# Kernel tuning notes

Measured on AMD Instinct MI355X. Metric: run time of the kernel, lower is better.

## Reference

```python
import jax, jax.numpy as jnp
import numpy as np

N_TYPES = 7
DT = 0.1
TAU_INIT = 20.0


def setup_inputs() -> dict:
    key = jax.random.key(0)
    k0, k1, k2, k3 = jax.random.split(key, 4)
    N = 49000          # n_neurons, divisible by 7 types
    E = 1_600_000      # n_edges (~avg degree 32)
    B = 8              # batch (via explicit v_init)
    n_tm1 = N // N_TYPES
    type_ids = (jnp.arange(N) % N_TYPES).astype(jnp.int32)   # type 0 == 'Tm1'
    tm1_indices = jnp.arange(0, N, N_TYPES, dtype=jnp.int32)  # positions where type_ids==0
    return {
        "tm1_input": jax.random.normal(k0, (B, n_tm1), jnp.float32),
        "v_init": jnp.zeros((B, N), jnp.float32),
        "weights": jax.random.normal(k1, (E,), jnp.float32),
        "bias": jnp.zeros((N,), jnp.float32),
        "tau_params": jnp.full((N_TYPES,), TAU_INIT, jnp.float32),
        "scale_excitatory": jnp.ones((), jnp.float32),
        "scale_inhibitory": jnp.ones((), jnp.float32),
        "source_indices": jax.random.randint(k2, (E,), 0, N, dtype=jnp.int32),
        "target_indices": jax.random.randint(k3, (E,), 0, N, dtype=jnp.int32),
        "type_ids": type_ids,
        "tm1_indices": tm1_indices,
        "steps": 100,
    }


def reference(tm1_input, v_init, weights, bias, tau_params,
              scale_excitatory, scale_inhibitory,
              source_indices, target_indices, type_ids, tm1_indices, steps):
    # per-neuron tau from per-type params (torch: get_tau_vector via masks)
    tau = tau_params[type_ids]                                   # [N]
    one = jnp.ones((), weights.dtype)
    edge_scales = jnp.where(weights > 0, scale_excitatory,
                            jnp.where(weights < 0, scale_inhibitory, one))
    scaled_weights = weights * edge_scales                       # [E]

    def step(v, _):
        v = v.at[:, tm1_indices].set(tm1_input)                  # clamp Tm1 neurons
        r = jax.nn.relu(v)                                       # activation
        edge_currents = r[:, source_indices] * scaled_weights    # gather [B,E]
        syn = jnp.zeros_like(v).at[:, target_indices].add(edge_currents)  # scatter-add [B,N]
        dv = (-v + syn + bias) / tau
        dv = dv.at[:, tm1_indices].set(0.0)                      # Tm1 held fixed
        return v + DT * dv, None

    v, _ = jax.lax.scan(step, v_init, None, length=steps)
    return v
```

## Files before the change

### kernel.cpp

```cpp
#include <hip/hip_runtime.h>


#define BLK 256
#define STEPS 100
#define NBATCH 8
#define PRE 6
#define NBUCK 256
#define CHUNK 4096
#define PERT 16
static constexpr float DT_C = 0.1f;

typedef unsigned uv4 __attribute__((ext_vector_type(4)));

__device__ __forceinline__ unsigned f2bf_rne(float x) {
    unsigned u = __float_as_uint(x);
    return (u + 0x7FFFu + ((u >> 16) & 1u)) >> 16;
}
__device__ __forceinline__ unsigned pk_bf2(float a, float b) {
    return f2bf_rne(a) | (f2bf_rne(b) << 16);
}

__global__ void k_zero(int* counts, int* countS, int* tm1_pos, int N) {
    int i = blockIdx.x * BLK + threadIdx.x;
    if (i < N) { counts[i] = 0; countS[i] = 0; tm1_pos[i] = -1; }
}

__global__ void k_tm1pos(const int* __restrict__ tm1_idx, int* tm1_pos, int NT) {
    int i = blockIdx.x * BLK + threadIdx.x;
    if (i < NT) tm1_pos[tm1_idx[i]] = i;
}

__global__ void k_hist(const int* __restrict__ srcI, const int* __restrict__ tgt,
                       const int* __restrict__ type_ids,
                       int* counts, int* countS, unsigned char* __restrict__ flagA,
                       int E) {
    int i = blockIdx.x * BLK + threadIdx.x;
    if (i >= E) return;
    int t = tgt[i];
    atomicAdd(&counts[t], 1);
    unsigned char st = (type_ids[srcI[i]] == 0) ? 1 : 0;
    if (st) atomicAdd(&countS[t], 1);
    flagA[i] = st;
}

__global__ void k_scan1(const int* __restrict__ counts, int* offsets, int* bsum, int N) {
    __shared__ int s[BLK];
    int tx = threadIdx.x;
    int i = blockIdx.x * BLK + tx;
    int v = (i < N) ? counts[i] : 0;
    s[tx] = v; __syncthreads();
    for (int d = 1; d < BLK; d <<= 1) {
        int t = (tx >= d) ? s[tx - d] : 0;
        __syncthreads();
        s[tx] += t;
        __syncthreads();
    }
    if (i < N) offsets[i] = s[tx] - v;
    if (tx == BLK - 1) bsum[blockIdx.x] = s[tx];
}

__global__ void k_scan2(int* bsum, int nb) {
    __shared__ int s[BLK];
    int tx = threadIdx.x;
    int v = (tx < nb) ? bsum[tx] : 0;
    s[tx] = v; __syncthreads();
    for (int d = 1; d < BLK; d <<= 1) {
        int t = (tx >= d) ? s[tx - d] : 0;
        __syncthreads();
        s[tx] += t;
        __syncthreads();
    }
    if (tx < nb) bsum[tx] = s[tx] - v;
}

__global__ void k_scan3(const int* __restrict__ bsum, int* offsets, int N, int E) {
    int i = blockIdx.x * BLK + threadIdx.x;
    if (i < N) offsets[i] += bsum[i >> 8];
    else if (i == N) offsets[N] = E;
}

__global__ void k_prep(const int* __restrict__ offsets, const int* __restrict__ countS,
                       int* dynEnd, int* gCursor, int N, int span) {
    int i = blockIdx.x * BLK + threadIdx.x;
    if (i < N) dynEnd[i] = offsets[i + 1] - countS[i];
    if (i < NBUCK) {
        int t0 = i * span; if (t0 > N) t0 = N;
        gCursor[i] = offsets[t0];
    }
}

__global__ __launch_bounds__(256) void k_bucket(
        const int* __restrict__ srcI, const int* __restrict__ tgtI,
        const float* __restrict__ w,
        const float* __restrict__ se, const float* __restrict__ si,
        const unsigned char* __restrict__ flagA,
        int* gCursor, unsigned long long* __restrict__ csr_tmp, int E, int span) {
    __shared__ unsigned long long stg[CHUNK];
    __shared__ int hcnt[NBUCK], hcur[NBUCK], hbase[NBUCK], gb[NBUCK], sc1[NBUCK];
    int base = blockIdx.x * CHUNK;
    int cnt = E - base; if (cnt > CHUNK) cnt = CHUNK;
    int tx = threadIdx.x;
    hcnt[tx] = 0;
    __syncthreads();

    float sE = se[0], sI = si[0];
    unsigned long long ent[PERT];
    int ebk[PERT];
    #pragma unroll
    for (int k = 0; k < PERT; ++k) {
        int o = k * 256 + tx;
        ent[k] = 0; ebk[k] = -1;
        if (o < cnt) {
            int i = base + o;
            int t = tgtI[i], s = srcI[i];
            float wv = w[i];
            float sc = wv > 0.f ? sE : (wv < 0.f ? sI : 1.f);
            unsigned wb = f2bf_rne(wv * sc);
            unsigned long long fl = flagA[i] ? (1ull << 63) : 0ull;
            ent[k] = (unsigned long long)(unsigned)t
                   | ((unsigned long long)(unsigned)s << 16)
                   | ((unsigned long long)wb << 32) | fl;
            int b = t / span;
            ebk[k] = b;
            atomicAdd(&hcnt[b], 1);
        }
    }
    __syncthreads();
    int v = hcnt[tx];
    sc1[tx] = v; __syncthreads();
    for (int d = 1; d < NBUCK; d <<= 1) {
        int t2 = (tx >= d) ? sc1[tx - d] : 0;
        __syncthreads();
        sc1[tx] += t2;
        __syncthreads();
    }
    hbase[tx] = sc1[tx] - v;
    hcur[tx]  = sc1[tx] - v;
    gb[tx] = atomicAdd(&gCursor[tx], v);
    __syncthreads();
    #pragma unroll
    for (int k = 0; k < PERT; ++k) {
        if (ebk[k] >= 0) {
            int r = atomicAdd(&hcur[ebk[k]], 1);
            stg[r] = ent[k];
        }
    }
    __syncthreads();
    for (int idx = tx; idx < cnt; idx += 256) {
        unsigned long long e = stg[idx];
        int b = (int)(e & 0xFFFFu) / span;
        csr_tmp[gb[b] + (idx - hbase[b])] = e;
    }
}

__global__ __launch_bounds__(256) void k_place(
        const int* __restrict__ offsets, const int* __restrict__ dynEnd,
        const unsigned long long* __restrict__ csr_tmp,
        unsigned* __restrict__ csr, int N, int span) {
    __shared__ int curD[256], curS[256];
    int b = blockIdx.x;
    int n0 = b * span;
    int nE = n0 + span; if (nE > N) nE = N;
    if (n0 >= N) return;
    int tx = threadIdx.x;
    for (int l = tx; l < nE - n0; l += 256) {
        curD[l] = offsets[n0 + l];
        curS[l] = dynEnd[n0 + l];
    }
    __syncthreads();
    int s = offsets[n0], e = offsets[nE];
    for (int i = s + tx; i < e; i += 256) {
        unsigned long long en = csr_tmp[i];
        int t = (int)(en & 0xFFFFu);
        int l = t - n0;
        int pos = (en >> 63) ? atomicAdd(&curS[l], 1) : atomicAdd(&curD[l], 1);
        unsigned src = (unsigned)((en >> 16) & 0xFFFFu);
        unsigned wb  = (unsigned)((en >> 32) & 0xFFFFu);
        csr[pos] = (wb << 16) | src;
    }
}

__global__ void k_initv(const float* __restrict__ tm1_in, const float* __restrict__ v_init,
                        const float* __restrict__ tau_p,
                        const int* __restrict__ type_ids, const int* __restrict__ tm1_pos,
                        float* __restrict__ v_w, uint4* __restrict__ r0, uint4* __restrict__ r1,
                        float2* __restrict__ coef2, int N, int NT) {
    int n = blockIdx.x * BLK + threadIdx.x;
    if (n >= N) return;
    int k = tm1_pos[n];
    float g = DT_C / tau_p[type_ids[n]];
    coef2[n] = make_float2((k >= 0) ? 0.f : (1.f - g), g);
    float vv[NBATCH], rr[NBATCH];
    for (int b = 0; b < NBATCH; ++b) {
        float val = (k >= 0) ? tm1_in[b * NT + k] : v_init[b * N + n];
        vv[b] = val;
        rr[b] = fmaxf(val, 0.f);
    }
    float4* vp = (float4*)(v_w + (size_t)n * 8);
    vp[0] = make_float4(vv[0], vv[1], vv[2], vv[3]);
    vp[1] = make_float4(vv[4], vv[5], vv[6], vv[7]);
    uint4 rq = make_uint4(pk_bf2(rr[0], rr[1]), pk_bf2(rr[2], rr[3]),
                          pk_bf2(rr[4], rr[5]), pk_bf2(rr[6], rr[7]));
    r0[n] = rq;
    r1[n] = rq;
}

__device__ __forceinline__ float butterfly8(float4 a0, float4 a1, int sub) {
    int bit0 = sub & 1, bit1 = (sub >> 1) & 1, bit2 = (sub >> 2) & 1;
    float b0 = (bit0 ? a0.y : a0.x) + __shfl_xor(bit0 ? a0.x : a0.y, 1);
    float b1 = (bit0 ? a0.w : a0.z) + __shfl_xor(bit0 ? a0.z : a0.w, 1);
    float b2 = (bit0 ? a1.y : a1.x) + __shfl_xor(bit0 ? a1.x : a1.y, 1);
    float b3 = (bit0 ? a1.w : a1.z) + __shfl_xor(bit0 ? a1.z : a1.w, 1);
    float c0 = (bit1 ? b1 : b0) + __shfl_xor(bit1 ? b0 : b1, 2);
    float c1 = (bit1 ? b3 : b2) + __shfl_xor(bit1 ? b2 : b3, 2);
    return (bit2 ? c1 : c0) + __shfl_xor(bit2 ? c0 : c1, 4);
}

__global__ void k_static(const int* __restrict__ offsets, const int* __restrict__ dynEnd,
                         const unsigned* __restrict__ csr, const uint4* __restrict__ r0,
                         const float2* __restrict__ coef2, const float* __restrict__ bias,
                         float* __restrict__ cF, int N) {
    int tid = blockIdx.x * BLK + threadIdx.x;
    int n = tid >> 3;
    int sub = threadIdx.x & 7;
    if (n >= N) return;
    float g = coef2[n].y;
    int s = dynEnd[n], e = offsets[n + 1];
    float4 a0 = make_float4(0.f, 0.f, 0.f, 0.f);
    float4 a1 = make_float4(0.f, 0.f, 0.f, 0.f);
    for (int i = s + sub; i < e; i += 8) {
        unsigned ew = csr[i];
        float w = __uint_as_float(ew & 0xFFFF0000u);
        uint4 q = r0[ew & 0xFFFFu];
        a0.x = fmaf(w, __uint_as_float(q.x << 16),          a0.x);
        a0.y = fmaf(w, __uint_as_float(q.x & 0xFFFF0000u),  a0.y);
        a0.z = fmaf(w, __uint_as_float(q.y << 16),          a0.z);
        a0.w = fmaf(w, __uint_as_float(q.y & 0xFFFF0000u),  a0.w);
        a1.x = fmaf(w, __uint_as_float(q.z << 16),          a1.x);
        a1.y = fmaf(w, __uint_as_float(q.z & 0xFFFF0000u),  a1.y);
        a1.z = fmaf(w, __uint_as_float(q.w << 16),          a1.z);
        a1.w = fmaf(w, __uint_as_float(q.w & 0xFFFF0000u),  a1.w);
    }
    float syn = butterfly8(a0, a1, sub);
    cF[(size_t)n * 8 + sub] = (syn + bias[n]) * g;
}

__global__ __launch_bounds__(BLK) void k_step(
        const int* __restrict__ offsets, const int* __restrict__ dynEnd,
        const unsigned* __restrict__ csr,
        const float2* __restrict__ coef2, const float* __restrict__ cF,
        const uv4* __restrict__ r_prev,
        float* __restrict__ v_w, unsigned short* __restrict__ r_next,
        float* __restrict__ out, int N) {
    int tid = blockIdx.x * BLK + threadIdx.x;
    int n = tid >> 3;
    int sub = threadIdx.x & 7;
    if (n >= N) return;
    float2 cf = coef2[n];
    size_t idx = (size_t)n * 8 + sub;
    if (cf.x == 0.f) {
        if (out) out[(size_t)sub * N + n] = v_w[idx];
        return;
    }
    int s = offsets[n], e = dynEnd[n];

    float wj[PRE];
    int   sj[PRE];
    #pragma unroll
    for (int j = 0; j < PRE; ++j) {
        int i2 = s + sub + 8 * j;
        unsigned ew = (i2 < e) ? __builtin_nontemporal_load(csr + i2) : 0u;
        wj[j] = __uint_as_float(ew & 0xFFFF0000u);
        sj[j] = (int)(ew & 0xFFFFu);
    }
    uv4 q[PRE];
    #pragma unroll
    for (int j = 0; j < PRE; ++j) {
        int i2 = s + sub + 8 * j;
        q[j] = (i2 < e) ? r_prev[sj[j]] : (uv4)(0u);
    }
    float4 a0 = make_float4(0.f, 0.f, 0.f, 0.f);
    float4 a1 = make_float4(0.f, 0.f, 0.f, 0.f);
    #pragma unroll
    for (int j = 0; j < PRE; ++j) {
        float w = wj[j];
        a0.x = fmaf(w, __uint_as_float(q[j].x << 16),          a0.x);
        a0.y = fmaf(w, __uint_as_float(q[j].x & 0xFFFF0000u),  a0.y);
        a0.z = fmaf(w, __uint_as_float(q[j].y << 16),          a0.z);
        a0.w = fmaf(w, __uint_as_float(q[j].y & 0xFFFF0000u),  a0.w);
        a1.x = fmaf(w, __uint_as_float(q[j].z << 16),          a1.x);
        a1.y = fmaf(w, __uint_as_float(q[j].z & 0xFFFF0000u),  a1.y);
        a1.z = fmaf(w, __uint_as_float(q[j].w << 16),          a1.z);
        a1.w = fmaf(w, __uint_as_float(q[j].w & 0xFFFF0000u),  a1.w);
    }
    for (int i2 = s + sub + 8 * PRE; i2 < e; i2 += 8) {
        unsigned ew = __builtin_nontemporal_load(csr + i2);
        float w = __uint_as_float(ew & 0xFFFF0000u);
        uv4 qq = r_prev[ew & 0xFFFFu];
        a0.x = fmaf(w, __uint_as_float(qq.x << 16),          a0.x);
        a0.y = fmaf(w, __uint_as_float(qq.x & 0xFFFF0000u),  a0.y);
        a0.z = fmaf(w, __uint_as_float(qq.y << 16),          a0.z);
        a0.w = fmaf(w, __uint_as_float(qq.y & 0xFFFF0000u),  a0.w);
        a1.x = fmaf(w, __uint_as_float(qq.z << 16),          a1.x);
        a1.y = fmaf(w, __uint_as_float(qq.z & 0xFFFF0000u),  a1.y);
        a1.z = fmaf(w, __uint_as_float(qq.w << 16),          a1.z);
        a1.w = fmaf(w, __uint_as_float(qq.w & 0xFFFF0000u),  a1.w);
    }
    float syn = butterfly8(a0, a1, sub);
    float vo = __builtin_nontemporal_load(v_w + idx);
    float cf3 = __builtin_nontemporal_load(cF + idx);
    float vn = vo * cf.x + syn * cf.y + cf3;
    if (out) {
        out[(size_t)sub * N + n] = vn;
    } else {
        __builtin_nontemporal_store(vn, v_w + idx);
        r_next[idx] = (unsigned short)f2bf_rne(fmaxf(vn, 0.f));
    }
}

static inline size_t align16(size_t x) { return (x + 15) & ~(size_t)15; }

extern "C" void kernel_launch(void* const* d_in, const int* in_sizes, int n_in,
                              void* d_out, int out_size, void* d_ws, size_t ws_size,
                              hipStream_t stream) {
    const float* tm1_in  = (const float*)d_in[0];
    const float* v_init  = (const float*)d_in[1];
    const float* weights = (const float*)d_in[2];
    const float* bias    = (const float*)d_in[3];
    const float* tau_p   = (const float*)d_in[4];
    const float* se      = (const float*)d_in[5];
    const float* si      = (const float*)d_in[6];
    const int*   srcI    = (const int*)d_in[7];
    const int*   tgtI    = (const int*)d_in[8];
    const int*   type_ids= (const int*)d_in[9];
    const int*   tm1_idx = (const int*)d_in[10];

    const int E  = in_sizes[2];
    const int N  = in_sizes[3];
    const int NT = in_sizes[10];
    const int span = (N + NBUCK - 1) / NBUCK;

    char* p = (char*)d_ws;
    size_t off = 0;
    auto take = [&](size_t bytes) { void* r = p + off; off += align16(bytes); return r; };
    int*      offsets = (int*)     take((size_t)(N + 1) * 4);
    int*      counts  = (int*)     take((size_t)N * 4);
    int*      countS  = (int*)     take((size_t)N * 4);
    int*      dynEnd  = (int*)     take((size_t)N * 4);
    int*      tm1_pos = (int*)     take((size_t)N * 4);
    int*      bsum    = (int*)     take(1024 * 4);
    int*      gCursor = (int*)     take(NBUCK * 4);
    unsigned char* flagA = (unsigned char*)take((size_t)E);
    unsigned* csr     = (unsigned*)take((size_t)E * 4);
    unsigned long long* csr_tmp = (unsigned long long*)take((size_t)E * 8);
    float2*   coef2   = (float2*)  take((size_t)N * 8);
    float*    cF      = (float*)   take((size_t)N * 8 * 4);
    float*    v_w     = (float*)   take((size_t)N * 8 * 4);
    uint4*    r0      = (uint4*)   take((size_t)N * 16);
    uint4*    r1      = (uint4*)   take((size_t)N * 16);
    (void)ws_size;

    const int gN  = (N + BLK - 1) / BLK;
    const int gN1 = (N + 1 + BLK - 1) / BLK;
    const int gE  = (E + BLK - 1) / BLK;
    const int gNT = (NT + BLK - 1) / BLK;
    const int g8  = (N * 8 + BLK - 1) / BLK;
    const int gCH = (E + CHUNK - 1) / CHUNK;

    k_zero<<<gN, BLK, 0, stream>>>(counts, countS, tm1_pos, N);
    k_tm1pos<<<gNT, BLK, 0, stream>>>(tm1_idx, tm1_pos, NT);
    k_hist<<<gE, BLK, 0, stream>>>(srcI, tgtI, type_ids, counts, countS, flagA, E);
    k_scan1<<<gN, BLK, 0, stream>>>(counts, offsets, bsum, N);
    k_scan2<<<1, BLK, 0, stream>>>(bsum, gN);
    k_scan3<<<gN1, BLK, 0, stream>>>(bsum, offsets, N, E);
    k_prep<<<gN, BLK, 0, stream>>>(offsets, countS, dynEnd, gCursor, N, span);
    k_bucket<<<gCH, 256, 0, stream>>>(srcI, tgtI, weights, se, si, flagA,
                                      gCursor, csr_tmp, E, span);
    k_place<<<NBUCK, 256, 0, stream>>>(offsets, dynEnd, csr_tmp, csr, N, span);
    k_initv<<<gN, BLK, 0, stream>>>(tm1_in, v_init, tau_p, type_ids, tm1_pos,
                                    v_w, r0, r1, coef2, N, NT);
    k_static<<<g8, BLK, 0, stream>>>(offsets, dynEnd, csr, r0, coef2, bias, cF, N);

    uint4* rb[2] = { r0, r1 };
    for (int s = 0; s < STEPS; ++s) {
        float* outp = (s == STEPS - 1) ? (float*)d_out : nullptr;
        k_step<<<g8, BLK, 0, stream>>>(offsets, dynEnd, csr, coef2, cF,
                                       (const uv4*)rb[s & 1], v_w,
                                       (unsigned short*)rb[(s + 1) & 1],
                                       outp, N);
    }
}
```

Measured before the change: 1.158 ms.

## Build CSR via bucket counts and per-bucket local scans instead of global histogram

Replaces the per-neuron global atomic histogram, the three-pass prefix scan and the prep kernel with a coarse per-bucket count using shared-memory histograms plus a single 256-entry scan. Per-neuron offsets and dynamic/static split points are now computed inside k_place from local shared-memory counts and scans. The Tm1-source flag is computed directly in k_bucket, so the flag array is gone. This cuts several kernel launches and about 1.6M global atomics from the setup phase, at the cost of reading csr_tmp twice in k_place. The 100-step loop is unchanged, so the effect is limited to setup.

```diff
diff --git a/kernel.cpp b/kernel.cpp
--- a/kernel.cpp
+++ b/kernel.cpp
@@ -20,9 +20,10 @@
     return f2bf_rne(a) | (f2bf_rne(b) << 16);
 }
 
-__global__ void k_zero(int* counts, int* countS, int* tm1_pos, int N) {
+__global__ void k_zero(int* tm1_pos, int* bcount, int N) {
     int i = blockIdx.x * BLK + threadIdx.x;
-    if (i < N) { counts[i] = 0; countS[i] = 0; tm1_pos[i] = -1; }
+    if (i < N) tm1_pos[i] = -1;
+    if (i < NBUCK) bcount[i] = 0;
 }
 
 __global__ void k_tm1pos(const int* __restrict__ tm1_idx, int* tm1_pos, int NT) {
@@ -30,70 +31,40 @@
     if (i < NT) tm1_pos[tm1_idx[i]] = i;
 }
 
-__global__ void k_hist(const int* __restrict__ srcI, const int* __restrict__ tgt,
-                       const int* __restrict__ type_ids,
-                       int* counts, int* countS, unsigned char* __restrict__ flagA,
-                       int E) {
-    int i = blockIdx.x * BLK + threadIdx.x;
-    if (i >= E) return;
-    int t = tgt[i];
-    atomicAdd(&counts[t], 1);
-    unsigned char st = (type_ids[srcI[i]] == 0) ? 1 : 0;
-    if (st) atomicAdd(&countS[t], 1);
-    flagA[i] = st;
-}
-
-__global__ void k_scan1(const int* __restrict__ counts, int* offsets, int* bsum, int N) {
-    __shared__ int s[BLK];
+__global__ __launch_bounds__(256) void k_bcount(const int* __restrict__ tgtI,
+                                                int* bcount, int E, int span) {
+    __shared__ int h[NBUCK];
     int tx = threadIdx.x;
-    int i = blockIdx.x * BLK + tx;
-    int v = (i < N) ? counts[i] : 0;
+    h[tx] = 0;
+    __syncthreads();
+    int base = blockIdx.x * CHUNK;
+    int cnt = E - base; if (cnt > CHUNK) cnt = CHUNK;
+    for (int o = tx; o < cnt; o += 256)
+        atomicAdd(&h[tgtI[base + o] / span], 1);
+    __syncthreads();
+    if (h[tx]) atomicAdd(&bcount[tx], h[tx]);
+}
+
+__global__ void k_bscan(const int* __restrict__ bcount, int* bbase, int* gCursor) {
+    __shared__ int s[NBUCK];
+    int tx = threadIdx.x;
+    int v = bcount[tx];
     s[tx] = v; __syncthreads();
-    for (int d = 1; d < BLK; d <<= 1) {
+    for (int d = 1; d < NBUCK; d <<= 1) {
         int t = (tx >= d) ? s[tx - d] : 0;
         __syncthreads();
         s[tx] += t;
         __syncthreads();
     }
-    if (i < N) offsets[i] = s[tx] - v;
-    if (tx == BLK - 1) bsum[blockIdx.x] = s[tx];
-}
-
-__global__ void k_scan2(int* bsum, int nb) {
-    __shared__ int s[BLK];
-    int tx = threadIdx.x;
-    int v = (tx < nb) ? bsum[tx] : 0;
-    s[tx] = v; __syncthreads();
-    for (int d = 1; d < BLK; d <<= 1) {
-        int t = (tx >= d) ? s[tx - d] : 0;
-        __syncthreads();
-        s[tx] += t;
-        __syncthreads();
-    }
-    if (tx < nb) bsum[tx] = s[tx] - v;
-}
-
-__global__ void k_scan3(const int* __restrict__ bsum, int* offsets, int N, int E) {
-    int i = blockIdx.x * BLK + threadIdx.x;
-    if (i < N) offsets[i] += bsum[i >> 8];
-    else if (i == N) offsets[N] = E;
-}
-
-__global__ void k_prep(const int* __restrict__ offsets, const int* __restrict__ countS,
-                       int* dynEnd, int* gCursor, int N, int span) {
-    int i = blockIdx.x * BLK + threadIdx.x;
-    if (i < N) dynEnd[i] = offsets[i + 1] - countS[i];
-    if (i < NBUCK) {
-        int t0 = i * span; if (t0 > N) t0 = N;
-        gCursor[i] = offsets[t0];
-    }
+    bbase[tx]   = s[tx] - v;
+    gCursor[tx] = s[tx] - v;
+    if (tx == NBUCK - 1) bbase[NBUCK] = s[tx];
 }
 
 __global__ __launch_bounds__(256) void k_bucket(
         const int* __restrict__ srcI, const int* __restrict__ tgtI,
-        const float* __restrict__ w,
+        const float* __restrict__ w, const int* __restrict__ type_ids,
         const float* __restrict__ se, const float* __restrict__ si,
-        const unsigned char* __restrict__ flagA,
         int* gCursor, unsigned long long* __restrict__ csr_tmp, int E, int span) {
     __shared__ unsigned long long stg[CHUNK];
     __shared__ int hcnt[NBUCK], hcur[NBUCK], hbase[NBUCK], gb[NBUCK], sc1[NBUCK];
@@ -116,7 +87,7 @@
             float wv = w[i];
             float sc = wv > 0.f ? sE : (wv < 0.f ? sI : 1.f);
             unsigned wb = f2bf_rne(wv * sc);
-            unsigned long long fl = flagA[i] ? (1ull << 63) : 0ull;
+            unsigned long long fl = (type_ids[s] == 0) ? (1ull << 63) : 0ull;
             ent[k] = (unsigned long long)(unsigned)t
                    | ((unsigned long long)(unsigned)s << 16)
                    | ((unsigned long long)wb << 32) | fl;
@@ -154,29 +125,48 @@
 }
 
 __global__ __launch_bounds__(256) void k_place(
-        const int* __restrict__ offsets, const int* __restrict__ dynEnd,
         const unsigned long long* __restrict__ csr_tmp,
-        unsigned* __restrict__ csr, int N, int span) {
-    __shared__ int curD[256], curS[256];
+        const int* __restrict__ bbase,
+        unsigned* __restrict__ csr, int* __restrict__ offsets,
+        int* __restrict__ dynEnd, int N, int E, int span) {
+    __shared__ int cntD[256], cntS[256], tb[256], curD[256], curS[256];
     int b = blockIdx.x;
     int n0 = b * span;
-    int nE = n0 + span; if (nE > N) nE = N;
-    if (n0 >= N) return;
+    int nT = N - n0; if (nT > span) nT = span;
     int tx = threadIdx.x;
-    for (int l = tx; l < nE - n0; l += 256) {
-        curD[l] = offsets[n0 + l];
-        curS[l] = dynEnd[n0 + l];
-    }
-    __syncthreads();
-    int s = offsets[n0], e = offsets[nE];
-    for (int i = s + tx; i < e; i += 256) {
+    cntD[tx] = 0; cntS[tx] = 0;
+    __syncthreads();
+    int rs = bbase[b], re = bbase[b + 1];
+    for (int i = rs + tx; i < re; i += 256) {
         unsigned long long en = csr_tmp[i];
-        int t = (int)(en & 0xFFFFu);
-        int l = t - n0;
+        int l = (int)(en & 0xFFFFu) - n0;
+        if (en >> 63) atomicAdd(&cntS[l], 1);
+        else          atomicAdd(&cntD[l], 1);
+    }
+    __syncthreads();
+    int tot = cntD[tx] + cntS[tx];
+    tb[tx] = tot; __syncthreads();
+    for (int d = 1; d < 256; d <<= 1) {
+        int t2 = (tx >= d) ? tb[tx - d] : 0;
+        __syncthreads();
+        tb[tx] += t2;
+        __syncthreads();
+    }
+    int obase = rs + tb[tx] - tot;
+    if (tx < nT) {
+        offsets[n0 + tx] = obase;
+        dynEnd[n0 + tx]  = obase + cntD[tx];
+        curD[tx] = obase;
+        curS[tx] = obase + cntD[tx];
+    }
+    if (b == NBUCK - 1 && tx == 0) offsets[N] = E;
+    __syncthreads();
+    for (int i = rs + tx; i < re; i += 256) {
+        unsigned long long en = csr_tmp[i];
+        int l = (int)(en & 0xFFFFu) - n0;
         int pos = (en >> 63) ? atomicAdd(&curS[l], 1) : atomicAdd(&curD[l], 1);
-        unsigned src = (unsigned)((en >> 16) & 0xFFFFu);
-        unsigned wb  = (unsigned)((en >> 32) & 0xFFFFu);
-        csr[pos] = (wb << 16) | src;
+        csr[pos] = ((unsigned)((en >> 32) & 0xFFFFu) << 16)
+                 | (unsigned)((en >> 16) & 0xFFFFu);
     }
 }
 
@@ -344,13 +334,11 @@
     size_t off = 0;
     auto take = [&](size_t bytes) { void* r = p + off; off += align16(bytes); return r; };
     int*      offsets = (int*)     take((size_t)(N + 1) * 4);
-    int*      counts  = (int*)     take((size_t)N * 4);
-    int*      countS  = (int*)     take((size_t)N * 4);
     int*      dynEnd  = (int*)     take((size_t)N * 4);
     int*      tm1_pos = (int*)     take((size_t)N * 4);
-    int*      bsum    = (int*)     take(1024 * 4);
+    int*      bcount  = (int*)     take(NBUCK * 4);
+    int*      bbase   = (int*)     take((NBUCK + 1) * 4);
     int*      gCursor = (int*)     take(NBUCK * 4);
-    unsigned char* flagA = (unsigned char*)take((size_t)E);
     unsigned* csr     = (unsigned*)take((size_t)E * 4);
     unsigned long long* csr_tmp = (unsigned long long*)take((size_t)E * 8);
     float2*   coef2   = (float2*)  take((size_t)N * 8);
@@ -361,22 +349,18 @@
     (void)ws_size;
 
     const int gN  = (N + BLK - 1) / BLK;
-    const int gN1 = (N + 1 + BLK - 1) / BLK;
-    const int gE  = (E + BLK - 1) / BLK;
     const int gNT = (NT + BLK - 1) / BLK;
     const int g8  = (N * 8 + BLK - 1) / BLK;
     const int gCH = (E + CHUNK - 1) / CHUNK;
 
-    k_zero<<<gN, BLK, 0, stream>>>(counts, countS, tm1_pos, N);
+    k_zero<<<gN, BLK, 0, stream>>>(tm1_pos, bcount, N);
     k_tm1pos<<<gNT, BLK, 0, stream>>>(tm1_idx, tm1_pos, NT);
-    k_hist<<<gE, BLK, 0, stream>>>(srcI, tgtI, type_ids, counts, countS, flagA, E);
-    k_scan1<<<gN, BLK, 0, stream>>>(counts, offsets, bsum, N);
-    k_scan2<<<1, BLK, 0, stream>>>(bsum, gN);
-    k_scan3<<<gN1, BLK, 0, stream>>>(bsum, offsets, N, E);
-    k_prep<<<gN, BLK, 0, stream>>>(offsets, countS, dynEnd, gCursor, N, span);
-    k_bucket<<<gCH, 256, 0, stream>>>(srcI, tgtI, weights, se, si, flagA,
+    k_bcount<<<gCH, 256, 0, stream>>>(tgtI, bcount, E, span);
+    k_bscan<<<1, NBUCK, 0, stream>>>(bcount, bbase, gCursor);
+    k_bucket<<<gCH, 256, 0, stream>>>(srcI, tgtI, weights, type_ids, se, si,
                                       gCursor, csr_tmp, E, span);
-    k_place<<<NBUCK, 256, 0, stream>>>(offsets, dynEnd, csr_tmp, csr, N, span);
+    k_place<<<NBUCK, 256, 0, stream>>>(csr_tmp, bbase, csr, offsets, dynEnd,
+                                       N, E, span);
     k_initv<<<gN, BLK, 0, stream>>>(tm1_in, v_init, tau_p, type_ids, tm1_pos,
                                     v_w, r0, r1, coef2, N, NT);
     k_static<<<g8, BLK, 0, stream>>>(offsets, dynEnd, csr, r0, coef2, bias, cF, N);
```

After: 1.073 ms. -7.3%, faster.
